# Kernel optimization log

Measured on AMD Instinct MI355X. Metric: run time of the kernel, lower is better.

Reference implementation:

```python
import jax, jax.numpy as jnp
import numpy as np

BATCH, SEQ, IN_DIM, HID, STATE, NLAYERS, OUT = 32, 2048, 32, 512, 64, 4, 2
EPS = 1e-5


def layer_norm(x, g, b):
    m = jnp.mean(x, axis=-1, keepdims=True)
    v = jnp.mean((x - m) ** 2, axis=-1, keepdims=True)
    return (x - m) / jnp.sqrt(v + EPS) * g + b


def s4_layer(x, A, C, D, g, b):
    # x: (B, L, H); A, C: (H, S); D: (H,)
    xn = layer_norm(x, g, b)
    u = jnp.swapaxes(xn, 0, 1)  # (L, B, H)

    def step(h, u_t):
        h = jnp.tanh(u_t @ A + h)          # (B, S)
        y = h @ C.T + u_t * D              # (B, H)
        return h, y

    h0 = jnp.zeros((x.shape[0], A.shape[1]), dtype=x.dtype)
    _, ys = jax.lax.scan(step, h0, u)
    return jnp.swapaxes(ys, 0, 1) + x      # residual


def setup_inputs() -> dict:
    key = jax.random.key(0)
    ks = jax.random.split(key, 16)
    s_in = 1.0 / np.sqrt(IN_DIM)
    s_h = 1.0 / np.sqrt(HID)
    s_h2 = 1.0 / np.sqrt(HID // 2)
    return {
        "x": jax.random.normal(ks[0], (BATCH, SEQ, IN_DIM), jnp.float32),
        "Win": jax.random.uniform(ks[1], (IN_DIM, HID), jnp.float32, -s_in, s_in),
        "bin_": jax.random.uniform(ks[2], (HID,), jnp.float32, -s_in, s_in),
        "A": jax.random.normal(ks[3], (NLAYERS, HID, STATE), jnp.float32) * 0.05,
        "C": jax.random.normal(ks[4], (NLAYERS, HID, STATE), jnp.float32) * 0.05,
        "Dvec": jax.random.normal(ks[5], (NLAYERS, HID), jnp.float32),
        "ln_g": jnp.ones((NLAYERS, HID), jnp.float32),
        "ln_b": jnp.zeros((NLAYERS, HID), jnp.float32),
        "norm_g": jnp.ones((HID,), jnp.float32),
        "norm_b": jnp.zeros((HID,), jnp.float32),
        "W1": jax.random.uniform(ks[6], (HID, HID // 2), jnp.float32, -s_h, s_h),
        "b1": jax.random.uniform(ks[7], (HID // 2,), jnp.float32, -s_h, s_h),
        "W2": jax.random.uniform(ks[8], (HID // 2, OUT), jnp.float32, -s_h2, s_h2),
        "b2": jax.random.uniform(ks[9], (OUT,), jnp.float32, -s_h2, s_h2),
    }


def reference(x, Win, bin_, A, C, Dvec, ln_g, ln_b, norm_g, norm_b, W1, b1, W2, b2):
    h = x @ Win + bin_                      # (B, L, H)
    for i in range(A.shape[0]):
        h = s4_layer(h, A[i], C[i], Dvec[i], ln_g[i], ln_b[i])
    h = layer_norm(h, norm_g, norm_b)
    h = h[:, -1, :]                         # last timestep
    h = jax.nn.gelu(h @ W1 + b1, approximate=False)  # torch nn.GELU uses erf
    return h @ W2 + b2
```

## Files before the change

### kernel.cpp

```cpp
#include <hip/hip_runtime.h>

#define BATCH   32
#define SEQ     2048
#define IN_DIM  32
#define HID     512
#define STATE   64
#define NLAYERS 4
#define NTOK    (BATCH*SEQ)
#define EPS     1e-5f
#define KTAN    2.8853900817779268f
#define NCHUNK  64
#define WARMUP  32

#define CF4(p) (*reinterpret_cast<const float4*>(p))

typedef __attribute__((ext_vector_type(8))) short short8v;
typedef __attribute__((ext_vector_type(4))) float f32x4;

__device__ __forceinline__ float fast_exp2(float x){ return __builtin_amdgcn_exp2f(x); }
__device__ __forceinline__ float fast_rcp(float x){ return __builtin_amdgcn_rcpf(x); }
__device__ __forceinline__ short f2bf(float f){
  unsigned u = __float_as_uint(f);
  unsigned r = (u + 0x7FFF + ((u>>16)&1)) >> 16;
  return (short)r;
}
__device__ __forceinline__ float bf2f(short s){
  return __uint_as_float(((unsigned)(unsigned short)s) << 16);
}

__global__ __launch_bounds__(256) void k_prep(
    const float* __restrict__ A, const float* __restrict__ g,
    const float* __restrict__ b, const float* __restrict__ Win,
    const float* __restrict__ bin, const float* __restrict__ C,
    short* __restrict__ ApT, float* __restrict__ GA, float* __restrict__ BA,
    short* __restrict__ WA1Th, short* __restrict__ WA1Tl,
    float* __restrict__ binA, short* __restrict__ Cb, short* __restrict__ WinT)
{
  __shared__ float red[4][64], red2[4][64];
  int tid = threadIdx.x;
  int s = tid & 63, part = tid >> 6;
  int blk = blockIdx.x;
  if (blk < NLAYERS){
    int l = blk;
    const float* Al = A + l*HID*STATE;
    const float* Cl = C + l*HID*STATE;
    const float* gl = g + l*HID;
    const float* bl = b + l*HID;
    float ga=0.f, ba=0.f;
    for (int j=part*128; j<(part+1)*128; ++j){
      float a  = Al[j*STATE+s];
      float ap = gl[j]*a;
      ApT[l*HID*STATE + s*HID + j] = f2bf(ap);
      Cb[l*HID*STATE + j*STATE + s] = f2bf(Cl[j*STATE+s]);
      ga += ap; ba = fmaf(bl[j], a, ba);
    }
    red[part][s]=ga; red2[part][s]=ba;
    __syncthreads();
    if (tid < 64){
      GA[l*STATE+s] = red[0][s]+red[1][s]+red[2][s]+red[3][s];
      BA[l*STATE+s] = red2[0][s]+red2[1][s]+red2[2][s]+red2[3][s];
    }
  } else if (blk < NLAYERS+32){
    int k = blk - NLAYERS;
    const float* w = Win + k*HID;
    float acc = 0.f;
    for (int j=part*128; j<(part+1)*128; ++j)
      acc = fmaf(w[j], g[j]*A[j*STATE+s], acc);
    red[part][s] = acc;
    __syncthreads();
    if (tid < 64){
      float v = red[0][s]+red[1][s]+red[2][s]+red[3][s];
      short hi = f2bf(v);
      WA1Th[s*IN_DIM + k] = hi;
      WA1Tl[s*IN_DIM + k] = f2bf(v - bf2f(hi));
    }
  } else if (blk == NLAYERS+32){
    float acc = 0.f;
    for (int j=part*128; j<(part+1)*128; ++j)
      acc = fmaf(bin[j], g[j]*A[j*STATE+s], acc);
    red[part][s] = acc;
    __syncthreads();
    if (tid < 64) binA[s] = red[0][s]+red[1][s]+red[2][s]+red[3][s];
  } else {
    for (int e = tid; e < HID*IN_DIM; e += 256){
      int cc = e >> 5, k = e & 31;
      WinT[cc*IN_DIM + k] = f2bf(Win[k*HID + cc]);
    }
  }
}

__global__ __launch_bounds__(256) void k_input(const float* __restrict__ x,
    const short* __restrict__ WinT, const float* __restrict__ bin,
    const short* __restrict__ WA1Th, const short* __restrict__ WA1Tl,
    const float* __restrict__ binA,
    const float* __restrict__ GA0, const float* __restrict__ BA0,
    short* __restrict__ h, _Float16* __restrict__ U, float2* __restrict__ stats)
{
  __shared__ __align__(16) short xhi[64][72];
  __shared__ __align__(16) short xlo[64][72];
  __shared__ __align__(16) short Ysh[2][64][76];
  __shared__ float2 statS[64];
  int m0 = blockIdx.x * 64;
  int tid = threadIdx.x;
  int w = tid >> 6, lane = tid & 63;
  int c = lane & 15, q = lane >> 4;
  int vrow = tid >> 3, vcb = tid & 7;
  #pragma unroll
  for (int i=0;i<8;i++){
    int idx = tid + i*256;
    int row = idx >> 5, k = idx & 31;
    float v = x[(size_t)(m0+row)*IN_DIM + k];
    short hi = f2bf(v);
    xhi[row][k] = hi;
    xlo[row][k] = f2bf(v - bf2f(hi));
  }
  __syncthreads();
  short8v ah = *reinterpret_cast<const short8v*>(&xhi[w*16 + c][q*8]);
  short8v al = *reinterpret_cast<const short8v*>(&xlo[w*16 + c][q*8]);
  float sum0=0.f, sq0=0.f, sum1=0.f, sq1=0.f;
  for (int jc=0; jc<HID; jc+=64){
    int cb = (jc >> 6) & 1;
    #pragma unroll
    for (int t=0;t<4;t++){
      short8v bv = *reinterpret_cast<const short8v*>(&WinT[(size_t)(jc + t*16 + c)*IN_DIM + q*8]);
      f32x4 a = {0.f,0.f,0.f,0.f};
      a = __builtin_amdgcn_mfma_f32_16x16x32_bf16(ah, bv, a, 0, 0, 0);
      int col = jc + t*16 + c;
      float bj = bin[col];
      #pragma unroll
      for (int r=0;r<4;r++)
        Ysh[cb][w*16 + q*4 + r][t*16 + c] = f2bf(a[r] + bj);
    }
    __syncthreads();
    #pragma unroll
    for (int rep=0; rep<2; ++rep){
      int row = vrow + rep*32;
      int m = m0 + row;
      short8v yv = *reinterpret_cast<const short8v*>(&Ysh[cb][row][vcb*8]);
      *reinterpret_cast<short8v*>(&h[(size_t)m*HID + jc + vcb*8]) = yv;
      float lsum=0.f, lsq=0.f;
      #pragma unroll
      for (int i=0;i<8;i++){
        float o = bf2f(yv[i]);
        lsum += o; lsq += o*o;
      }
      if (rep) { sum1 += lsum; sq1 += lsq; } else { sum0 += lsum; sq0 += lsq; }
    }
  }
  #pragma unroll
  for (int off=1; off<8; off<<=1){
    sum0 += __shfl_xor(sum0, off);  sq0 += __shfl_xor(sq0, off);
    sum1 += __shfl_xor(sum1, off);  sq1 += __shfl_xor(sq1, off);
  }
  if (vcb == 0){
    float m0v = sum0*(1.f/HID);
    float v0 = sq0*(1.f/HID) - m0v*m0v;
    float2 s0 = make_float2(m0v, rsqrtf(fmaxf(v0,0.f)+EPS));
    stats[m0 + vrow] = s0;  statS[vrow] = s0;
    float m1v = sum1*(1.f/HID);
    float v1 = sq1*(1.f/HID) - m1v*m1v;
    float2 s1 = make_float2(m1v, rsqrtf(fmaxf(v1,0.f)+EPS));
    stats[m0 + 32 + vrow] = s1;  statS[32 + vrow] = s1;
  }
  __syncthreads();
  float mu[4], rs[4];
  #pragma unroll
  for (int r=0;r<4;r++){
    float2 s2 = statS[w*16 + q*4 + r];
    mu[r]=s2.x; rs[r]=s2.y;
  }
  #pragma unroll
  for (int t=0;t<4;t++){
    short8v bh  = *reinterpret_cast<const short8v*>(&WA1Th[(size_t)(t*16 + c)*IN_DIM + q*8]);
    short8v blv = *reinterpret_cast<const short8v*>(&WA1Tl[(size_t)(t*16 + c)*IN_DIM + q*8]);
    f32x4 a = {0.f,0.f,0.f,0.f};
    a = __builtin_amdgcn_mfma_f32_16x16x32_bf16(ah, bh, a, 0, 0, 0);
    a = __builtin_amdgcn_mfma_f32_16x16x32_bf16(al, bh, a, 0, 0, 0);
    a = __builtin_amdgcn_mfma_f32_16x16x32_bf16(ah, blv, a, 0, 0, 0);
    int s = t*16 + c;
    float ga = GA0[s], ba = BA0[s], bA = binA[s];
    #pragma unroll
    for (int r=0;r<4;r++){
      int m = m0 + w*16 + q*4 + r;
      float u = a[r] + bA;
      U[(size_t)m*STATE + s] = (_Float16)fmaf(KTAN, rs[r]*(u - mu[r]*ga) + ba, KTAN);
    }
  }
}

__global__ __launch_bounds__(256) void k_ugemm(const short* __restrict__ hb,
    const float2* __restrict__ stats, const short* __restrict__ ApT,
    const float* __restrict__ GA, const float* __restrict__ BA,
    _Float16* __restrict__ U)
{
  __shared__ __align__(16) short Hsh[2][64][72];
  __shared__ __align__(16) short Bsh[2][64][72];
  int m0 = blockIdx.x * 64;
  int tid = threadIdx.x;
  int w = tid >> 6, lane = tid & 63;
  int c = lane & 15, q = lane >> 4;
  float mu[4], rs[4];
  #pragma unroll
  for (int r=0;r<4;r++){
    float2 s2 = stats[m0 + w*16 + q*4 + r];
    mu[r]=s2.x; rs[r]=s2.y;
  }
  #pragma unroll
  for (int p=0;p<2;p++){
    int idx = tid + p*256;
    int row = idx >> 3, kb = idx & 7;
    *reinterpret_cast<short8v*>(&Hsh[0][row][kb*8]) =
      *reinterpret_cast<const short8v*>(&hb[(size_t)(m0+row)*HID + kb*8]);
    *reinterpret_cast<short8v*>(&Bsh[0][row][kb*8]) =
      *reinterpret_cast<const short8v*>(&ApT[(size_t)row*HID + kb*8]);
  }
  __syncthreads();
  f32x4 acc[4] = {{0.f,0.f,0.f,0.f},{0.f,0.f,0.f,0.f},{0.f,0.f,0.f,0.f},{0.f,0.f,0.f,0.f}};
  #pragma unroll
  for (int i=0;i<8;i++){
    int cb = i & 1;
    if (i < 7){
      int kc = (i+1)*64;
      #pragma unroll
      for (int p=0;p<2;p++){
        int idx = tid + p*256;
        int row = idx >> 3, kb = idx & 7;
        *reinterpret_cast<short8v*>(&Hsh[cb^1][row][kb*8]) =
          *reinterpret_cast<const short8v*>(&hb[(size_t)(m0+row)*HID + kc + kb*8]);
        *reinterpret_cast<short8v*>(&Bsh[cb^1][row][kb*8]) =
          *reinterpret_cast<const short8v*>(&ApT[(size_t)row*HID + kc + kb*8]);
      }
    }
    short8v a0 = *reinterpret_cast<const short8v*>(&Hsh[cb][w*16 + c][q*8]);
    short8v a1 = *reinterpret_cast<const short8v*>(&Hsh[cb][w*16 + c][32 + q*8]);
    #pragma unroll
    for (int t=0;t<4;t++){
      short8v b0 = *reinterpret_cast<const short8v*>(&Bsh[cb][t*16 + c][q*8]);
      short8v b1 = *reinterpret_cast<const short8v*>(&Bsh[cb][t*16 + c][32 + q*8]);
      acc[t] = __builtin_amdgcn_mfma_f32_16x16x32_bf16(a0, b0, acc[t], 0, 0, 0);
      acc[t] = __builtin_amdgcn_mfma_f32_16x16x32_bf16(a1, b1, acc[t], 0, 0, 0);
    }
    __syncthreads();
  }
  #pragma unroll
  for (int t=0;t<4;t++){
    int s = t*16 + c;
    float ga = GA[s], ba = BA[s];
    #pragma unroll
    for (int r=0;r<4;r++){
      int m = m0 + w*16 + q*4 + r;
      U[(size_t)m*STATE + s] = (_Float16)fmaf(KTAN, rs[r]*(acc[t][r] - mu[r]*ga) + ba, KTAN);
    }
  }
}

__global__ __launch_bounds__(64) void k_scan(const _Float16* __restrict__ U,
                                             short* __restrict__ H)
{
  int b = blockIdx.x >> 6;
  int p = blockIdx.x & 63;
  int s = threadIdx.x;
  const _Float16* Ub = U + (size_t)b*SEQ*STATE + s;
  short* Hb = H + (size_t)b*SEQ*STATE + s;
  float r = 0.5f;
  float cur[32], nxt[32];
  int t = (p == 0) ? 0 : (p*32 - WARMUP);
  int nsub = (p == 0) ? 1 : 2;
  #pragma unroll
  for (int i=0;i<32;i++) cur[i] = (float)Ub[(t+i)*STATE];
  for (int cidx=0; cidx<nsub; ++cidx){
    bool has_next = (cidx+1 < nsub);
    if (has_next){
      #pragma unroll
      for (int i=0;i<32;i++) nxt[i] = (float)Ub[(t+32+i)*STATE];
    }
    if ((p == 0) || (cidx > 0)){
      #pragma unroll
      for (int i=0;i<32;i++){
        float e = fast_exp2(fmaf(-2.f*KTAN, r, cur[i]));
        r = fast_rcp(1.f + e);
        Hb[(t+i)*STATE] = f2bf(fmaf(-2.f, r, 1.f));
      }
    } else {
      #pragma unroll
      for (int i=0;i<32;i++){
        float e = fast_exp2(fmaf(-2.f*KTAN, r, cur[i]));
        r = fast_rcp(1.f + e);
      }
    }
    if (has_next){
      #pragma unroll
      for (int i=0;i<32;i++) cur[i] = nxt[i];
    }
    t += 32;
  }
}

__global__ __launch_bounds__(256) void k_yep4(
    short* __restrict__ h, const short* __restrict__ Hg,
    const short* __restrict__ Cb, const float* __restrict__ Dl,
    const float* __restrict__ gl, const float* __restrict__ bl,
    const float2* __restrict__ stats_in, float2* __restrict__ stats_out)
{
  __shared__ __align__(16) short Hsh[64][72];
  __shared__ __align__(16) short Csh[64][72];
  __shared__ __align__(16) short Ysh[64][76];
  int m0 = blockIdx.x * 64;
  int tid = threadIdx.x;
  int w = tid >> 6, lane = tid & 63;
  int c = lane & 15, q = lane >> 4;
  int vrow = tid >> 3;
  int vcb  = tid & 7;
  #pragma unroll
  for (int p=0;p<2;p++){
    int idx = tid + p*256;
    int row = idx >> 3, kb = idx & 7;
    *reinterpret_cast<short8v*>(&Hsh[row][kb*8]) =
      *reinterpret_cast<const short8v*>(&Hg[(size_t)(m0+row)*STATE + kb*8]);
  }
  float2 sin0 = stats_in[m0 + vrow];
  float2 sin1 = stats_in[m0 + 32 + vrow];
  float sum0=0.f, sq0=0.f, sum1=0.f, sq1=0.f;
  __syncthreads();
  short8v a0 = *reinterpret_cast<const short8v*>(&Hsh[w*16 + c][q*8]);
  short8v a1 = *reinterpret_cast<const short8v*>(&Hsh[w*16 + c][32 + q*8]);
  for (int jc=0; jc<HID; jc+=64){
    #pragma unroll
    for (int p=0;p<2;p++){
      int idx = tid + p*256;
      int col = idx >> 3, kb = idx & 7;
      *reinterpret_cast<short8v*>(&Csh[col][kb*8]) =
        *reinterpret_cast<const short8v*>(&Cb[(size_t)(jc+col)*STATE + kb*8]);
    }
    __syncthreads();
    #pragma unroll
    for (int t=0;t<4;t++){
      short8v b0 = *reinterpret_cast<const short8v*>(&Csh[t*16 + c][q*8]);
      short8v b1 = *reinterpret_cast<const short8v*>(&Csh[t*16 + c][32 + q*8]);
      f32x4 a = {0.f,0.f,0.f,0.f};
      a = __builtin_amdgcn_mfma_f32_16x16x32_bf16(a0, b0, a, 0, 0, 0);
      a = __builtin_amdgcn_mfma_f32_16x16x32_bf16(a1, b1, a, 0, 0, 0);
      #pragma unroll
      for (int r=0;r<4;r++)
        Ysh[w*16 + q*4 + r][t*16 + c] = f2bf(a[r]);
    }
    __syncthreads();
    int col0 = jc + vcb*8;
    float4 gA = CF4(&gl[col0]), gB = CF4(&gl[col0+4]);
    float4 bA = CF4(&bl[col0]), bB = CF4(&bl[col0+4]);
    float4 dA = CF4(&Dl[col0]), dB = CF4(&Dl[col0+4]);
    float ga[8] = {gA.x,gA.y,gA.z,gA.w,gB.x,gB.y,gB.z,gB.w};
    float ba[8] = {bA.x,bA.y,bA.z,bA.w,bB.x,bB.y,bB.z,bB.w};
    float da[8] = {dA.x,dA.y,dA.z,dA.w,dB.x,dB.y,dB.z,dB.w};
    #pragma unroll
    for (int rep=0; rep<2; ++rep){
      int row = vrow + rep*32;
      int m = m0 + row;
      float mu_ = rep ? sin1.x : sin0.x;
      float rs_ = rep ? sin1.y : sin0.y;
      short8v hv = *reinterpret_cast<const short8v*>(&h[(size_t)m*HID + col0]);
      short8v yv = *reinterpret_cast<const short8v*>(&Ysh[row][vcb*8]);
      short8v ov;
      float lsum=0.f, lsq=0.f;
      #pragma unroll
      for (int i=0;i<8;i++){
        float hvf = bf2f(hv[i]);
        float o = hvf + bf2f(yv[i]) + fmaf((hvf-mu_)*rs_, ga[i], ba[i])*da[i];
        ov[i] = f2bf(o);
        lsum += o; lsq += o*o;
      }
      *reinterpret_cast<short8v*>(&h[(size_t)m*HID + col0]) = ov;
      if (rep) { sum1 += lsum; sq1 += lsq; } else { sum0 += lsum; sq0 += lsq; }
    }
  }
  #pragma unroll
  for (int off=1; off<8; off<<=1){
    sum0 += __shfl_xor(sum0, off);  sq0 += __shfl_xor(sq0, off);
    sum1 += __shfl_xor(sum1, off);  sq1 += __shfl_xor(sq1, off);
  }
  if (vcb == 0){
    float m0v = sum0*(1.f/HID);
    float v0 = sq0*(1.f/HID) - m0v*m0v;
    stats_out[m0 + vrow] = make_float2(m0v, rsqrtf(fmaxf(v0,0.f)+EPS));
    float m1v = sum1*(1.f/HID);
    float v1 = sq1*(1.f/HID) - m1v*m1v;
    stats_out[m0 + 32 + vrow] = make_float2(m1v, rsqrtf(fmaxf(v1,0.f)+EPS));
  }
}

__global__ __launch_bounds__(256) void k_head(const short* __restrict__ h,
   const float2* __restrict__ stats, const float* __restrict__ ng, const float* __restrict__ nb,
   const float* __restrict__ W1, const float* __restrict__ b1,
   const float* __restrict__ W2, const float* __restrict__ b2,
   float* __restrict__ out)
{
  int bb = blockIdx.x;
  int m = bb*SEQ + (SEQ-1);
  int tid = threadIdx.x;
  __shared__ float xs[HID];
  __shared__ float red[8];
  float2 st = stats[m];
  #pragma unroll
  for (int i=0;i<2;i++){
    int j = tid + i*256;
    float v = bf2f(h[(size_t)m*HID + j]);
    xs[j] = fmaf((v - st.x)*st.y, ng[j], nb[j]);
  }
  __syncthreads();
  float acc = b1[tid];
  #pragma unroll 8
  for (int j=0;j<HID;j++) acc = fmaf(xs[j], W1[j*(HID/2) + tid], acc);
  float ge = 0.5f*acc*(1.f + erff(acc*0.70710678118654752f));
  float p0 = ge*W2[tid*2+0];
  float p1 = ge*W2[tid*2+1];
  #pragma unroll
  for (int off=32; off; off>>=1){ p0 += __shfl_down(p0, off); p1 += __shfl_down(p1, off); }
  int wid = tid>>6;
  if ((tid&63)==0){ red[wid*2]=p0; red[wid*2+1]=p1; }
  __syncthreads();
  if (tid==0){
    float o0=b2[0], o1=b2[1];
    #pragma unroll
    for (int w=0;w<4;w++){ o0+=red[w*2]; o1+=red[w*2+1]; }
    out[bb*2+0]=o0; out[bb*2+1]=o1;
  }
}

extern "C" void kernel_launch(void* const* d_in, const int* in_sizes, int n_in,
                              void* d_out, int out_size, void* d_ws, size_t ws_size,
                              hipStream_t stream)
{
  (void)in_sizes; (void)n_in; (void)out_size; (void)ws_size;
  const float* x   = (const float*)d_in[0];
  const float* Win = (const float*)d_in[1];
  const float* bin = (const float*)d_in[2];
  const float* A   = (const float*)d_in[3];
  const float* C   = (const float*)d_in[4];
  const float* Dv  = (const float*)d_in[5];
  const float* lng = (const float*)d_in[6];
  const float* lnb = (const float*)d_in[7];
  const float* ng  = (const float*)d_in[8];
  const float* nb  = (const float*)d_in[9];
  const float* W1  = (const float*)d_in[10];
  const float* b1  = (const float*)d_in[11];
  const float* W2  = (const float*)d_in[12];
  const float* b2  = (const float*)d_in[13];
  float* out = (float*)d_out;
  char* ws = (char*)d_ws;
  short*     hb   = (short*)(ws + 0);
  _Float16*  Ubuf = (_Float16*)(ws + (size_t)67108864);
  short*     Hbuf = (short*)(ws + (size_t)83886080);
  float2*    st0  = (float2*)(ws + (size_t)92274688);
  float2*    st1  = (float2*)(ws + (size_t)92798976);
  short*     ApT  = (short*)(ws + (size_t)93323264);
  float*     GAb  = (float*)(ws + (size_t)93585408);
  float*     BAb  = (float*)(ws + (size_t)93586432);
  float*     binAb= (float*)(ws + (size_t)93587456);
  short*     Cb   = (short*)(ws + (size_t)93587712);
  short*     WinT = (short*)(ws + (size_t)93849856);
  short*     WA1Th= (short*)(ws + (size_t)93882624);
  short*     WA1Tl= (short*)(ws + (size_t)93886720);

  hipLaunchKernelGGL(k_prep,  dim3(38), dim3(256), 0, stream,
      A, lng, lnb, Win, bin, C, ApT, GAb, BAb, WA1Th, WA1Tl, binAb, Cb, WinT);
  hipLaunchKernelGGL(k_input, dim3(NTOK/64), dim3(256), 0, stream,
      x, WinT, bin, WA1Th, WA1Tl, binAb, GAb, BAb, hb, Ubuf, st0);
  float2* scur = st0; float2* snxt = st1;
  for (int l=0; l<NLAYERS; ++l){
    if (l > 0){
      hipLaunchKernelGGL(k_ugemm, dim3(NTOK/64), dim3(256), 0, stream,
          hb, scur, ApT + l*HID*STATE, GAb + l*STATE, BAb + l*STATE, Ubuf);
    }
    hipLaunchKernelGGL(k_scan, dim3(BATCH*NCHUNK), dim3(64), 0, stream, Ubuf, Hbuf);
    hipLaunchKernelGGL(k_yep4, dim3(NTOK/64), dim3(256), 0, stream,
        hb, Hbuf, Cb + l*HID*STATE, Dv + l*HID, lng + l*HID, lnb + l*HID, scur, snxt);
    float2* t = scur; scur = snxt; snxt = t;
  }
  hipLaunchKernelGGL(k_head, dim3(BATCH), dim3(256), 0, stream,
      hb, scur, ng, nb, W1, b1, W2, b2, out);
}
```

Measured before the change: 244.1 us.

## Fuse next-layer U GEMM into the output/residual kernel epilogue

Removes the separate k_ugemm launch. The y/residual kernel now reuses its freshly computed bf16 output tile from shared memory as the A operand for the next layer's projection onto A. The U values are accumulated chunk by chunk and normalized with the row statistics the same block just computed. This avoids re-reading the whole hidden activation from global memory and saves one launch per layer. In exchange the fused kernel needs more shared memory, extra syncs and more accumulator registers, which may lower occupancy.

Measured after the change: 267.5 us. 1.1x slower.

```diff
diff --git a/kernel.cpp b/kernel.cpp
--- a/kernel.cpp
+++ b/kernel.cpp
@@ -188,72 +188,6 @@
   }
 }
 
-__global__ __launch_bounds__(256) void k_ugemm(const short* __restrict__ hb,
-    const float2* __restrict__ stats, const short* __restrict__ ApT,
-    const float* __restrict__ GA, const float* __restrict__ BA,
-    _Float16* __restrict__ U)
-{
-  __shared__ __align__(16) short Hsh[2][64][72];
-  __shared__ __align__(16) short Bsh[2][64][72];
-  int m0 = blockIdx.x * 64;
-  int tid = threadIdx.x;
-  int w = tid >> 6, lane = tid & 63;
-  int c = lane & 15, q = lane >> 4;
-  float mu[4], rs[4];
-  #pragma unroll
-  for (int r=0;r<4;r++){
-    float2 s2 = stats[m0 + w*16 + q*4 + r];
-    mu[r]=s2.x; rs[r]=s2.y;
-  }
-  #pragma unroll
-  for (int p=0;p<2;p++){
-    int idx = tid + p*256;
-    int row = idx >> 3, kb = idx & 7;
-    *reinterpret_cast<short8v*>(&Hsh[0][row][kb*8]) =
-      *reinterpret_cast<const short8v*>(&hb[(size_t)(m0+row)*HID + kb*8]);
-    *reinterpret_cast<short8v*>(&Bsh[0][row][kb*8]) =
-      *reinterpret_cast<const short8v*>(&ApT[(size_t)row*HID + kb*8]);
-  }
-  __syncthreads();
-  f32x4 acc[4] = {{0.f,0.f,0.f,0.f},{0.f,0.f,0.f,0.f},{0.f,0.f,0.f,0.f},{0.f,0.f,0.f,0.f}};
-  #pragma unroll
-  for (int i=0;i<8;i++){
-    int cb = i & 1;
-    if (i < 7){
-      int kc = (i+1)*64;
-      #pragma unroll
-      for (int p=0;p<2;p++){
-        int idx = tid + p*256;
-        int row = idx >> 3, kb = idx & 7;
-        *reinterpret_cast<short8v*>(&Hsh[cb^1][row][kb*8]) =
-          *reinterpret_cast<const short8v*>(&hb[(size_t)(m0+row)*HID + kc + kb*8]);
-        *reinterpret_cast<short8v*>(&Bsh[cb^1][row][kb*8]) =
-          *reinterpret_cast<const short8v*>(&ApT[(size_t)row*HID + kc + kb*8]);
-      }
-    }
-    short8v a0 = *reinterpret_cast<const short8v*>(&Hsh[cb][w*16 + c][q*8]);
-    short8v a1 = *reinterpret_cast<const short8v*>(&Hsh[cb][w*16 + c][32 + q*8]);
-    #pragma unroll
-    for (int t=0;t<4;t++){
-      short8v b0 = *reinterpret_cast<const short8v*>(&Bsh[cb][t*16 + c][q*8]);
-      short8v b1 = *reinterpret_cast<const short8v*>(&Bsh[cb][t*16 + c][32 + q*8]);
-      acc[t] = __builtin_amdgcn_mfma_f32_16x16x32_bf16(a0, b0, acc[t], 0, 0, 0);
-      acc[t] = __builtin_amdgcn_mfma_f32_16x16x32_bf16(a1, b1, acc[t], 0, 0, 0);
-    }
-    __syncthreads();
-  }
-  #pragma unroll
-  for (int t=0;t<4;t++){
-    int s = t*16 + c;
-    float ga = GA[s], ba = BA[s];
-    #pragma unroll
-    for (int r=0;r<4;r++){
-      int m = m0 + w*16 + q*4 + r;
-      U[(size_t)m*STATE + s] = (_Float16)fmaf(KTAN, rs[r]*(acc[t][r] - mu[r]*ga) + ba, KTAN);
-    }
-  }
-}
-
 __global__ __launch_bounds__(64) void k_scan(const _Float16* __restrict__ U,
                                              short* __restrict__ H)
 {
@@ -296,15 +230,19 @@
   }
 }
 
-__global__ __launch_bounds__(256) void k_yep4(
+__global__ __launch_bounds__(256) void k_yep7(
     short* __restrict__ h, const short* __restrict__ Hg,
     const short* __restrict__ Cb, const float* __restrict__ Dl,
     const float* __restrict__ gl, const float* __restrict__ bl,
-    const float2* __restrict__ stats_in, float2* __restrict__ stats_out)
+    const float2* __restrict__ stats_in, float2* __restrict__ stats_out,
+    const short* __restrict__ ApTn, const float* __restrict__ GAn,
+    const float* __restrict__ BAn, _Float16* __restrict__ U, int has_next)
 {
   __shared__ __align__(16) short Hsh[64][72];
   __shared__ __align__(16) short Csh[64][72];
+  __shared__ __align__(16) short Ash[64][72];
   __shared__ __align__(16) short Ysh[64][76];
+  __shared__ float2 statS[64];
   int m0 = blockIdx.x * 64;
   int tid = threadIdx.x;
   int w = tid >> 6, lane = tid & 63;
@@ -321,6 +259,8 @@
   float2 sin0 = stats_in[m0 + vrow];
   float2 sin1 = stats_in[m0 + 32 + vrow];
   float sum0=0.f, sq0=0.f, sum1=0.f, sq1=0.f;
+  f32x4 uacc[4] = {{0.f,0.f,0.f,0.f},{0.f,0.f,0.f,0.f},
+                   {0.f,0.f,0.f,0.f},{0.f,0.f,0.f,0.f}};
   __syncthreads();
   short8v a0 = *reinterpret_cast<const short8v*>(&Hsh[w*16 + c][q*8]);
   short8v a1 = *reinterpret_cast<const short8v*>(&Hsh[w*16 + c][32 + q*8]);
@@ -328,9 +268,18 @@
     #pragma unroll
     for (int p=0;p<2;p++){
       int idx = tid + p*256;
-      int col = idx >> 3, kb = idx & 7;
-      *reinterpret_cast<short8v*>(&Csh[col][kb*8]) =
-        *reinterpret_cast<const short8v*>(&Cb[(size_t)(jc+col)*STATE + kb*8]);
+      int row = idx >> 3, kb = idx & 7;
+      *reinterpret_cast<short8v*>(&Csh[row][kb*8]) =
+        *reinterpret_cast<const short8v*>(&Cb[(size_t)(jc+row)*STATE + kb*8]);
+    }
+    if (has_next){
+      #pragma unroll
+      for (int p=0;p<2;p++){
+        int idx = tid + p*256;
+        int row = idx >> 3, kb = idx & 7;
+        *reinterpret_cast<short8v*>(&Ash[row][kb*8]) =
+          *reinterpret_cast<const short8v*>(&ApTn[(size_t)row*HID + jc + kb*8]);
+      }
     }
     __syncthreads();
     #pragma unroll
@@ -370,8 +319,22 @@
         lsum += o; lsq += o*o;
       }
       *reinterpret_cast<short8v*>(&h[(size_t)m*HID + col0]) = ov;
+      *reinterpret_cast<short8v*>(&Ysh[row][vcb*8]) = ov;
       if (rep) { sum1 += lsum; sq1 += lsq; } else { sum0 += lsum; sq0 += lsq; }
     }
+    __syncthreads();
+    if (has_next){
+      short8v u0 = *reinterpret_cast<const short8v*>(&Ysh[w*16 + c][q*8]);
+      short8v u1 = *reinterpret_cast<const short8v*>(&Ysh[w*16 + c][32 + q*8]);
+      #pragma unroll
+      for (int t=0;t<4;t++){
+        short8v b0 = *reinterpret_cast<const short8v*>(&Ash[t*16 + c][q*8]);
+        short8v b1 = *reinterpret_cast<const short8v*>(&Ash[t*16 + c][32 + q*8]);
+        uacc[t] = __builtin_amdgcn_mfma_f32_16x16x32_bf16(u0, b0, uacc[t], 0, 0, 0);
+        uacc[t] = __builtin_amdgcn_mfma_f32_16x16x32_bf16(u1, b1, uacc[t], 0, 0, 0);
+      }
+    }
+    __syncthreads();
   }
   #pragma unroll
   for (int off=1; off<8; off<<=1){
@@ -381,10 +344,30 @@
   if (vcb == 0){
     float m0v = sum0*(1.f/HID);
     float v0 = sq0*(1.f/HID) - m0v*m0v;
-    stats_out[m0 + vrow] = make_float2(m0v, rsqrtf(fmaxf(v0,0.f)+EPS));
+    float2 s0 = make_float2(m0v, rsqrtf(fmaxf(v0,0.f)+EPS));
+    stats_out[m0 + vrow] = s0;  statS[vrow] = s0;
     float m1v = sum1*(1.f/HID);
     float v1 = sq1*(1.f/HID) - m1v*m1v;
-    stats_out[m0 + 32 + vrow] = make_float2(m1v, rsqrtf(fmaxf(v1,0.f)+EPS));
+    float2 s1 = make_float2(m1v, rsqrtf(fmaxf(v1,0.f)+EPS));
+    stats_out[m0 + 32 + vrow] = s1;  statS[32 + vrow] = s1;
+  }
+  if (!has_next) return;
+  __syncthreads();
+  float mu2[4], rs2[4];
+  #pragma unroll
+  for (int r=0;r<4;r++){
+    float2 s2 = statS[w*16 + q*4 + r];
+    mu2[r]=s2.x; rs2[r]=s2.y;
+  }
+  #pragma unroll
+  for (int t=0;t<4;t++){
+    int s = t*16 + c;
+    float ga = GAn[s], ba = BAn[s];
+    #pragma unroll
+    for (int r=0;r<4;r++){
+      int m = m0 + w*16 + q*4 + r;
+      U[(size_t)m*STATE + s] = (_Float16)fmaf(KTAN, rs2[r]*(uacc[t][r] - mu2[r]*ga) + ba, KTAN);
+    }
   }
 }
 
@@ -467,13 +450,13 @@
       x, WinT, bin, WA1Th, WA1Tl, binAb, GAb, BAb, hb, Ubuf, st0);
   float2* scur = st0; float2* snxt = st1;
   for (int l=0; l<NLAYERS; ++l){
-    if (l > 0){
-      hipLaunchKernelGGL(k_ugemm, dim3(NTOK/64), dim3(256), 0, stream,
-          hb, scur, ApT + l*HID*STATE, GAb + l*STATE, BAb + l*STATE, Ubuf);
-    }
+    int has_next = (l < NLAYERS-1) ? 1 : 0;
+    int ln = has_next ? (l+1) : 0;
     hipLaunchKernelGGL(k_scan, dim3(BATCH*NCHUNK), dim3(64), 0, stream, Ubuf, Hbuf);
-    hipLaunchKernelGGL(k_yep4, dim3(NTOK/64), dim3(256), 0, stream,
-        hb, Hbuf, Cb + l*HID*STATE, Dv + l*HID, lng + l*HID, lnb + l*HID, scur, snxt);
+    hipLaunchKernelGGL(k_yep7, dim3(NTOK/64), dim3(256), 0, stream,
+        hb, Hbuf, Cb + l*HID*STATE, Dv + l*HID, lng + l*HID, lnb + l*HID,
+        scur, snxt, ApT + ln*HID*STATE, GAb + ln*STATE, BAb + ln*STATE,
+        Ubuf, has_next);
     float2* t = scur; scur = snxt; snxt = t;
   }
   hipLaunchKernelGGL(k_head, dim3(BATCH), dim3(256), 0, stream,
```
